# Performance work log

Measured on AMD Instinct MI355X. Metric: run time of the kernel, lower is better.

## Reference

```python
import jax, jax.numpy as jnp
import numpy as np

FP32_MIN_NORMAL = 2.0 ** -126
BLOCK = 128
STD_DEV = 2.0
# inlier format int4: ebits=0, mbits=4+2, emax=0, max_norm=(2^5-1)/2^4
EBITS_IN, MBITS_IN, EMAX_IN, MAXNORM_IN = 0, 6, 0, (2 ** 5 - 1) / 2 ** 4
# outlier format fp8_e4m3: ebits=4, mbits=3+2, emax=2^3, max_norm=2^8*1.75
EBITS_OUT, MBITS_OUT, EMAX_OUT, MAXNORM_OUT = 4, 5, 8, 448.0
SCALE_EMAX = 2 ** (8 - 1) - 1  # inlier/outlier scale_bits = 8
SCALE_LO = -20.0  # original: lower clamp is -20 because -scale_emax < -20


def setup_inputs():
    key = jax.random.key(0)
    x = jax.random.normal(key, (4096, 8192), dtype=jnp.float32)
    return {"x": x}


def _quantize_elemwise(A, mbits, ebits, max_norm):
    # faithful to microxcaling _quantize_elemwise_core with allow_denorm=True,
    # saturate_normals=True, round='nearest' (finite inputs assumed)
    if ebits != 0:
        pexp = jnp.floor(jnp.log2(jnp.abs(A) + (A == 0).astype(A.dtype)))
        pexp = jnp.maximum(pexp, float(-(2 ** (ebits - 1)) + 2))
        scale = jnp.exp2(float(mbits - 2) - pexp)
    else:
        scale = float(2 ** (mbits - 2))
    out = A * scale
    out = jnp.sign(out) * jnp.floor(jnp.abs(out) + 0.5)  # round-to-nearest
    out = out / scale
    return jnp.clip(out, -max_norm, max_norm)


def _shared_exp(A):
    # max-abs over the block axis, then floor(log2(.)), zero-safe
    m = jnp.max(jnp.abs(A), axis=-1, keepdims=True)
    return jnp.floor(jnp.log2(m + FP32_MIN_NORMAL * (m == 0).astype(m.dtype)))


def _clamp_scale(se):
    se = jnp.where(se > SCALE_EMAX, jnp.nan, se)  # never triggers for fp32-range data
    return jnp.where(se < -SCALE_EMAX, SCALE_LO, se)


def _quantize_mx_outlier(x):
    R, C = x.shape  # C divisible by BLOCK -> no padding branch
    A = x.reshape(R, C // BLOCK, BLOCK)
    # outlier detection: mean/std of |A| per block (population std), bounds vs A
    absA = jnp.abs(A)
    mean = jnp.mean(absA, axis=-1, keepdims=True)
    std = jnp.sqrt(jnp.mean((absA - mean) ** 2, axis=-1, keepdims=True))
    outlier = ((A < mean - STD_DEV * std) | (A > mean + STD_DEV * std)).astype(A.dtype)
    inlier_val = A * (1.0 - outlier)
    outlier_val = A * outlier
    # inlier shared exponent + quantize
    se_in = _clamp_scale(_shared_exp(inlier_val) - EMAX_IN)
    s_in = jnp.exp2(se_in)
    inlier_val = _quantize_elemwise(inlier_val / s_in, MBITS_IN, EBITS_IN, MAXNORM_IN) * s_in
    # outlier path (note: scaled UP by inlier scale, as in original)
    outlier_val = outlier_val * s_in
    se_out = _clamp_scale(_shared_exp(outlier_val) - EMAX_OUT)
    s_out = jnp.exp2(se_out)
    outlier_val = _quantize_elemwise(outlier_val / s_out, MBITS_OUT, EBITS_OUT, MAXNORM_OUT) * s_out / s_in
    return (inlier_val + outlier_val).reshape(R, C)


def reference(x):
    return _quantize_mx_outlier(x)
```

## Files before the change

### kernel.cpp

```cpp
#include <hip/hip_runtime.h>

typedef float f32x4 __attribute__((ext_vector_type(4)));

#define DPP_X1 0xB1
#define DPP_X2 0x4E
#define DPP_R4 0x124
#define DPP_R8 0x128

template <int CTRL>
__device__ __forceinline__ float dpp_mv(float v) {
    return __int_as_float(__builtin_amdgcn_update_dpp(0, __float_as_int(v), CTRL, 0xF, 0xF, true));
}
template <int CTRL>
__device__ __forceinline__ double dpp_mv64(double v) {
    unsigned long long u = __double_as_longlong(v);
    int lo = __builtin_amdgcn_update_dpp(0, (int)(unsigned)(u & 0xFFFFFFFFull), CTRL, 0xF, 0xF, true);
    int hi = __builtin_amdgcn_update_dpp(0, (int)(unsigned)(u >> 32), CTRL, 0xF, 0xF, true);
    return __longlong_as_double(((unsigned long long)(unsigned)hi << 32) | (unsigned)lo);
}

__device__ __forceinline__ int flog2_exact(float x) {
    unsigned b = __float_as_uint(x);
    int e = (int)((b >> 23) & 0xFFu);
    if (e == 0) {
        unsigned m = b & 0x7FFFFFu;
        return 31 - __clz(m) - 149;
    }
    return e - 127;
}

__global__ __launch_bounds__(256) void mxq_kernel(const f32x4* __restrict__ x,
                                                  f32x4* __restrict__ y,
                                                  int ntask) {
    const int lane = threadIdx.x & 63;
    const int wid  = blockIdx.x * (blockDim.x >> 6) + (threadIdx.x >> 6);
    if (wid >= ntask) return;

    const size_t base = (size_t)wid * 128 + (lane >> 4) * 32 + (lane & 15);
    const f32x4 v0 = x[base];
    const f32x4 v1 = x[base + 16];
    float a[8] = {v0.x, v0.y, v0.z, v0.w, v1.x, v1.y, v1.z, v1.w};
    float ab[8];

    float s = 0.0f, s2 = 0.0f;
    #pragma unroll
    for (int i = 0; i < 8; ++i) {
        ab[i] = fabsf(a[i]);
        s += ab[i];
        s2 = fmaf(a[i], a[i], s2);
    }
    s += dpp_mv<DPP_X1>(s);  s2 += dpp_mv<DPP_X1>(s2);
    s += dpp_mv<DPP_X2>(s);  s2 += dpp_mv<DPP_X2>(s2);
    s += dpp_mv<DPP_R4>(s);  s2 += dpp_mv<DPP_R4>(s2);
    s += dpp_mv<DPP_R8>(s);  s2 += dpp_mv<DPP_R8>(s2);

    const float meanf = s * (1.0f / 128.0f);
    const float ms2   = s2 * (1.0f / 128.0f);
    float varf = fmaf(meanf, -meanf, ms2);
    varf = varf < 0.0f ? 0.0f : varf;
    const float thrf  = 2.0f * sqrtf(varf);
    const float delta = sqrtf(ms2) * 1.220703125e-4f;
    bool unc = (varf < ms2 * 2.44140625e-4f);

    bool o[8];
    #pragma unroll
    for (int i = 0; i < 8; ++i) {
        float w = fabsf(a[i] - meanf) - thrf;
        o[i] = w > 0.0f;
        unc = unc || (fabsf(w) < delta);
    }

    if (__any((int)unc)) {
        double sd = 0.0, sd2 = 0.0;
        double ad[8];
        #pragma unroll
        for (int i = 0; i < 8; ++i) {
            ad[i] = (double)a[i];
            sd += fabs(ad[i]);
            sd2 = fma(ad[i], ad[i], sd2);
        }
        sd += dpp_mv64<DPP_X1>(sd);  sd2 += dpp_mv64<DPP_X1>(sd2);
        sd += dpp_mv64<DPP_X2>(sd);  sd2 += dpp_mv64<DPP_X2>(sd2);
        sd += dpp_mv64<DPP_R4>(sd);  sd2 += dpp_mv64<DPP_R4>(sd2);
        sd += dpp_mv64<DPP_R8>(sd);  sd2 += dpp_mv64<DPP_R8>(sd2);
        const double meand = sd * (1.0 / 128.0);
        double vard = fma(meand, -meand, sd2 * (1.0 / 128.0));
        vard = vard < 0.0 ? 0.0 : vard;
        const double thrd = 2.0 * sqrt(vard);
        #pragma unroll
        for (int i = 0; i < 8; ++i)
            o[i] = fabs((double)a[i] - meand) > thrd;
    }

    float mi = 0.0f, mov = 0.0f;
    #pragma unroll
    for (int i = 0; i < 8; ++i) {
        mi  = fmaxf(mi,  o[i] ? 0.0f : ab[i]);
        mov = fmaxf(mov, o[i] ? ab[i] : 0.0f);
    }
    mi = fmaxf(mi, dpp_mv<DPP_X1>(mi));  mov = fmaxf(mov, dpp_mv<DPP_X1>(mov));
    mi = fmaxf(mi, dpp_mv<DPP_X2>(mi));  mov = fmaxf(mov, dpp_mv<DPP_X2>(mov));
    mi = fmaxf(mi, dpp_mv<DPP_R4>(mi));  mov = fmaxf(mov, dpp_mv<DPP_R4>(mov));
    mi = fmaxf(mi, dpp_mv<DPP_R8>(mi));  mov = fmaxf(mov, dpp_mv<DPP_R8>(mov));

    int se_in = (mi == 0.0f) ? -126 : flog2_exact(mi);
    if (se_in < -127) se_in = -20;
    int se_out = ((mov == 0.0f) ? -126 : (flog2_exact(mov) + se_in)) - 8;
    if (se_out < -127) se_out = -20;
    const int d    = se_in - se_out;
    const int g_in = se_in - 4;
    const int m9   = -(d + 9);
    const float L_in  = ldexpf(31.0f, g_in);
    const float L_out = ldexpf(448.0f, -d);

    f32x4 r0, r1;
    #pragma unroll
    for (int i = 0; i < 8; ++i) {
        int eb = (int)((__float_as_uint(a[i]) >> 23) & 0xFFu);
        int g_out = max(eb - 130, m9);
        int g = o[i] ? g_out : g_in;
        float t2 = ldexpf(a[i], -g);
        float r  = copysignf(truncf(fabsf(t2) + 0.5f), a[i]);
        float outv = ldexpf(r, g);
        float L = o[i] ? L_out : L_in;
        outv = __builtin_amdgcn_fmed3f(outv, -L, L);
        if (i < 4) r0[i] = outv; else r1[i - 4] = outv;
    }

    y[base]      = r0;
    y[base + 16] = r1;
}

extern "C" void kernel_launch(void* const* d_in, const int* in_sizes, int n_in,
                              void* d_out, int out_size, void* d_ws, size_t ws_size,
                              hipStream_t stream) {
    const f32x4* x = (const f32x4*)d_in[0];
    f32x4* y = (f32x4*)d_out;
    int n = in_sizes[0];
    int ntask = n / 512;
    int threads = 256;
    int waves_per_wg = threads / 64;
    int grid = (ntask + waves_per_wg - 1) / waves_per_wg;
    mxq_kernel<<<grid, threads, 0, stream>>>(x, y, ntask);
}
```

Before: 43.32 us.

## Process 16 elements per lane with 8-lane block groups

Each wave now handles 8 blocks instead of 4, so each lane holds 16 elements across four 16-byte loads and stores. The per-block reduction spans 8 lanes and finishes with two DPP steps plus one xor shuffle, replacing the two row-rotate DPP steps. The uncertainty test is rewritten as a two-sided comparison against precomputed bounds. The aim is more memory-level parallelism per thread and fewer reduction instructions per element, at the cost of more registers and half as many waves.

```diff
diff --git a/kernel.cpp b/kernel.cpp
--- a/kernel.cpp
+++ b/kernel.cpp
@@ -4,8 +4,6 @@
 
 #define DPP_X1 0xB1
 #define DPP_X2 0x4E
-#define DPP_R4 0x124
-#define DPP_R8 0x128
 
 template <int CTRL>
 __device__ __forceinline__ float dpp_mv(float v) {
@@ -31,28 +29,28 @@
 
 __global__ __launch_bounds__(256) void mxq_kernel(const f32x4* __restrict__ x,
                                                   f32x4* __restrict__ y,
-                                                  int ntask) {
+                                                  int nwave) {
     const int lane = threadIdx.x & 63;
     const int wid  = blockIdx.x * (blockDim.x >> 6) + (threadIdx.x >> 6);
-    if (wid >= ntask) return;
+    if (wid >= nwave) return;
 
-    const size_t base = (size_t)wid * 128 + (lane >> 4) * 32 + (lane & 15);
-    const f32x4 v0 = x[base];
-    const f32x4 v1 = x[base + 16];
-    float a[8] = {v0.x, v0.y, v0.z, v0.w, v1.x, v1.y, v1.z, v1.w};
-    float ab[8];
+    const size_t u0 = (size_t)wid * 256 + (lane >> 3) * 32 + (lane & 7);
+    const f32x4 v0 = x[u0];
+    const f32x4 v1 = x[u0 + 8];
+    const f32x4 v2 = x[u0 + 16];
+    const f32x4 v3 = x[u0 + 24];
+    float a[16] = {v0.x, v0.y, v0.z, v0.w, v1.x, v1.y, v1.z, v1.w,
+                   v2.x, v2.y, v2.z, v2.w, v3.x, v3.y, v3.z, v3.w};
 
     float s = 0.0f, s2 = 0.0f;
     #pragma unroll
-    for (int i = 0; i < 8; ++i) {
-        ab[i] = fabsf(a[i]);
-        s += ab[i];
+    for (int i = 0; i < 16; ++i) {
+        s += fabsf(a[i]);
         s2 = fmaf(a[i], a[i], s2);
     }
     s += dpp_mv<DPP_X1>(s);  s2 += dpp_mv<DPP_X1>(s2);
     s += dpp_mv<DPP_X2>(s);  s2 += dpp_mv<DPP_X2>(s2);
-    s += dpp_mv<DPP_R4>(s);  s2 += dpp_mv<DPP_R4>(s2);
-    s += dpp_mv<DPP_R8>(s);  s2 += dpp_mv<DPP_R8>(s2);
+    s += __shfl_xor(s, 4);   s2 += __shfl_xor(s2, 4);
 
     const float meanf = s * (1.0f / 128.0f);
     const float ms2   = s2 * (1.0f / 128.0f);
@@ -60,48 +58,48 @@
     varf = varf < 0.0f ? 0.0f : varf;
     const float thrf  = 2.0f * sqrtf(varf);
     const float delta = sqrtf(ms2) * 1.220703125e-4f;
+    const float thrlo = thrf - delta;
+    const float thrhi = thrf + delta;
     bool unc = (varf < ms2 * 2.44140625e-4f);
 
-    bool o[8];
+    bool o[16];
     #pragma unroll
-    for (int i = 0; i < 8; ++i) {
-        float w = fabsf(a[i] - meanf) - thrf;
-        o[i] = w > 0.0f;
-        unc = unc || (fabsf(w) < delta);
+    for (int i = 0; i < 16; ++i) {
+        float dd = fabsf(a[i] - meanf);
+        o[i] = dd > thrf;
+        unc = unc || (dd > thrlo && dd < thrhi);
     }
 
     if (__any((int)unc)) {
         double sd = 0.0, sd2 = 0.0;
-        double ad[8];
         #pragma unroll
-        for (int i = 0; i < 8; ++i) {
-            ad[i] = (double)a[i];
-            sd += fabs(ad[i]);
-            sd2 = fma(ad[i], ad[i], sd2);
+        for (int i = 0; i < 16; ++i) {
+            double ad = (double)a[i];
+            sd += fabs(ad);
+            sd2 = fma(ad, ad, sd2);
         }
         sd += dpp_mv64<DPP_X1>(sd);  sd2 += dpp_mv64<DPP_X1>(sd2);
         sd += dpp_mv64<DPP_X2>(sd);  sd2 += dpp_mv64<DPP_X2>(sd2);
-        sd += dpp_mv64<DPP_R4>(sd);  sd2 += dpp_mv64<DPP_R4>(sd2);
-        sd += dpp_mv64<DPP_R8>(sd);  sd2 += dpp_mv64<DPP_R8>(sd2);
+        sd += __shfl_xor(sd, 4);     sd2 += __shfl_xor(sd2, 4);
         const double meand = sd * (1.0 / 128.0);
         double vard = fma(meand, -meand, sd2 * (1.0 / 128.0));
         vard = vard < 0.0 ? 0.0 : vard;
         const double thrd = 2.0 * sqrt(vard);
         #pragma unroll
-        for (int i = 0; i < 8; ++i)
+        for (int i = 0; i < 16; ++i)
             o[i] = fabs((double)a[i] - meand) > thrd;
     }
 
     float mi = 0.0f, mov = 0.0f;
     #pragma unroll
-    for (int i = 0; i < 8; ++i) {
-        mi  = fmaxf(mi,  o[i] ? 0.0f : ab[i]);
-        mov = fmaxf(mov, o[i] ? ab[i] : 0.0f);
+    for (int i = 0; i < 16; ++i) {
+        float ab = fabsf(a[i]);
+        mi  = fmaxf(mi,  o[i] ? 0.0f : ab);
+        mov = fmaxf(mov, o[i] ? ab : 0.0f);
     }
     mi = fmaxf(mi, dpp_mv<DPP_X1>(mi));  mov = fmaxf(mov, dpp_mv<DPP_X1>(mov));
     mi = fmaxf(mi, dpp_mv<DPP_X2>(mi));  mov = fmaxf(mov, dpp_mv<DPP_X2>(mov));
-    mi = fmaxf(mi, dpp_mv<DPP_R4>(mi));  mov = fmaxf(mov, dpp_mv<DPP_R4>(mov));
-    mi = fmaxf(mi, dpp_mv<DPP_R8>(mi));  mov = fmaxf(mov, dpp_mv<DPP_R8>(mov));
+    mi = fmaxf(mi, __shfl_xor(mi, 4));   mov = fmaxf(mov, __shfl_xor(mov, 4));
 
     int se_in = (mi == 0.0f) ? -126 : flog2_exact(mi);
     if (se_in < -127) se_in = -20;
@@ -113,9 +111,9 @@
     const float L_in  = ldexpf(31.0f, g_in);
     const float L_out = ldexpf(448.0f, -d);
 
-    f32x4 r0, r1;
+    f32x4 r0, r1, r2, r3;
     #pragma unroll
-    for (int i = 0; i < 8; ++i) {
+    for (int i = 0; i < 16; ++i) {
         int eb = (int)((__float_as_uint(a[i]) >> 23) & 0xFFu);
         int g_out = max(eb - 130, m9);
         int g = o[i] ? g_out : g_in;
@@ -124,11 +122,16 @@
         float outv = ldexpf(r, g);
         float L = o[i] ? L_out : L_in;
         outv = __builtin_amdgcn_fmed3f(outv, -L, L);
-        if (i < 4) r0[i] = outv; else r1[i - 4] = outv;
+        if      (i < 4)  r0[i]      = outv;
+        else if (i < 8)  r1[i - 4]  = outv;
+        else if (i < 12) r2[i - 8]  = outv;
+        else             r3[i - 12] = outv;
     }
 
-    y[base]      = r0;
-    y[base + 16] = r1;
+    y[u0]      = r0;
+    y[u0 + 8]  = r1;
+    y[u0 + 16] = r2;
+    y[u0 + 24] = r3;
 }
 
 extern "C" void kernel_launch(void* const* d_in, const int* in_sizes, int n_in,
@@ -137,9 +140,9 @@
     const f32x4* x = (const f32x4*)d_in[0];
     f32x4* y = (f32x4*)d_out;
     int n = in_sizes[0];
-    int ntask = n / 512;
+    int nwave = n / 1024;
     int threads = 256;
     int waves_per_wg = threads / 64;
-    int grid = (ntask + waves_per_wg - 1) / waves_per_wg;
-    mxq_kernel<<<grid, threads, 0, stream>>>(x, y, ntask);
+    int grid = (nwave + waves_per_wg - 1) / waves_per_wg;
+    mxq_kernel<<<grid, threads, 0, stream>>>(x, y, nwave);
 }
```

After: 45.29 us. 1.05x slower.
